# Kernel tuning notes

Measured on AMD Instinct MI355X. Metric: run time of the kernel, lower is better.

Reference implementation:

```python
import jax, jax.numpy as jnp
import numpy as np
import math

N, D_MODEL, H = 2048, 1024, 16
DK = D_MODEL // H
EPS = 1e-5


def setup_inputs() -> dict:
    key = jax.random.key(0)
    ks = jax.random.split(key, 10)
    s = 0.05  # scale to keep attention logits in a sane range
    return {
        "x": jax.random.normal(ks[0], (N, D_MODEL), jnp.float32),
        "wq": jax.random.normal(ks[1], (H * D_MODEL, DK), jnp.float32) * s,
        "q_bias": jax.random.normal(ks[2], (H, DK), jnp.float32) * s,
        "wk": jax.random.normal(ks[3], (H * D_MODEL, DK), jnp.float32) * s,
        "k_bias": jax.random.normal(ks[4], (H, DK), jnp.float32) * s,
        "wv": jax.random.normal(ks[5], (H * D_MODEL, DK), jnp.float32) * s,
        "v_bias": jax.random.normal(ks[6], (H, DK), jnp.float32) * s,
        "wo": jax.random.normal(ks[7], (D_MODEL, D_MODEL), jnp.float32) * s,
        "o_bias": jax.random.normal(ks[8], (D_MODEL,), jnp.float32) * s,
        "alpha": jnp.ones((D_MODEL,), jnp.float32),
        "beta": jnp.zeros((D_MODEL,), jnp.float32),
        "n": N,
        "d_model": D_MODEL,
        "h": H,
    }


def reference(x, wq, q_bias, wk, k_bias, wv, v_bias, wo, o_bias, alpha, beta, n, d_model, h):
    dk = d_model // h
    # per-head weight slices wq[i*d_model:(i+1)*d_model] -> [h, d_model, dk]
    wq3 = wq.reshape(h, d_model, dk)
    wk3 = wk.reshape(h, d_model, dk)
    wv3 = wv.reshape(h, d_model, dk)
    q = jnp.einsum('nd,hdk->hnk', x, wq3) + q_bias[:, None, :]  # [h,n,dk]
    k = jnp.einsum('nd,hdk->hnk', x, wk3) + k_bias[:, None, :]
    v = jnp.einsum('nd,hdk->hnk', x, wv3) + v_bias[:, None, :]
    scores = jnp.einsum('hnk,hmk->hnm', q, k) / math.sqrt(dk)  # [h,n,n]
    attn = jax.nn.softmax(scores, axis=-1)  # dim=1 of 2D [n,n] == last dim
    heads = jnp.einsum('hnm,hmk->hnk', attn, v)  # [h,n,dk]
    concat = heads.transpose(1, 0, 2).reshape(n, d_model)  # [n, d_model]
    out = concat @ wo + o_bias + x  # out-proj + residual
    mu = jnp.mean(out, axis=-1, keepdims=True)
    var = jnp.mean(jnp.square(out - mu), axis=-1, keepdims=True)
    return alpha * (out - mu) / jnp.sqrt(var + EPS) + beta
```

## Files before the change

kernel.cpp:

```cpp
#include <hip/hip_runtime.h>


#define NN 2048
#define DM 1024
#define NH 16
#define DKH 64

typedef __attribute__((ext_vector_type(4))) float f32x4;
typedef __attribute__((ext_vector_type(8))) __bf16 bf16x8;
typedef __attribute__((ext_vector_type(4))) __bf16 bf16x4;

#define AS1 __attribute__((address_space(1)))
#define AS3 __attribute__((address_space(3)))
#define GLOAD16(g, l) __builtin_amdgcn_global_load_lds((const AS1 void*)(g), (AS3 void*)(l), 16, 0, 0)

static __device__ __forceinline__ f32x4 mfma16(bf16x8 a, bf16x8 b, f32x4 c) {
  return __builtin_amdgcn_mfma_f32_16x16x32_bf16(a, b, c, 0, 0, 0);
}

static __device__ __forceinline__ bf16x8 cat44(bf16x4 a, bf16x4 b) {
  bf16x8 r;
  r[0] = a[0]; r[1] = a[1]; r[2] = a[2]; r[3] = a[3];
  r[4] = b[0]; r[5] = b[1]; r[6] = b[2]; r[7] = b[3];
  return r;
}

__global__ __launch_bounds__(256) void cvt_all(const float* __restrict__ x,
                                               const float* __restrict__ wq,
                                               const float* __restrict__ wk,
                                               const float* __restrict__ wv,
                                               const float* __restrict__ wo,
                                               __bf16* __restrict__ x_bf,
                                               __bf16* __restrict__ wqkv_t,
                                               __bf16* __restrict__ wo_t) {
  const int b = blockIdx.x, t = threadIdx.x;
  if (b < 1024) {
    int i = (b * 256 + t) * 8;
    float4 a = *(const float4*)(x + i);
    float4 c = *(const float4*)(x + i + 4);
    bf16x8 o;
    o[0] = (__bf16)a.x; o[1] = (__bf16)a.y; o[2] = (__bf16)a.z; o[3] = (__bf16)a.w;
    o[4] = (__bf16)c.x; o[5] = (__bf16)c.y; o[6] = (__bf16)c.z; o[7] = (__bf16)c.w;
    *(bf16x8*)(x_bf + i) = o;
  } else if (b < 2560) {
    int bb = b - 1024;
    int c = (bb % 12) * 256 + t;
    int oct = bb / 12;
    const float* src = (c < 1024) ? wq : (c < 2048 ? wk : wv);
    int hk = c & 1023;
    int hh = hk >> 6, dkk = hk & 63;
    bf16x8 o;
#pragma unroll
    for (int j = 0; j < 8; ++j)
      o[j] = (__bf16)src[(hh * 1024 + oct * 8 + j) * 64 + dkk];
    *(bf16x8*)(wqkv_t + c * 1024 + oct * 8) = o;
  } else {
    int bb = b - 2560;
    int c = (bb % 4) * 256 + t;
    int oct = bb / 4;
    bf16x8 o;
#pragma unroll
    for (int j = 0; j < 8; ++j)
      o[j] = (__bf16)wo[(oct * 8 + j) * 1024 + c];
    *(bf16x8*)(wo_t + c * 1024 + oct * 8) = o;
  }
}

__global__ __launch_bounds__(256) void gemm_qkv(const __bf16* __restrict__ A,
                                                const __bf16* __restrict__ Bt,
                                                const float* __restrict__ biasq,
                                                const float* __restrict__ biask,
                                                const float* __restrict__ biasv,
                                                __bf16* __restrict__ Qo,
                                                __bf16* __restrict__ Ko,
                                                __bf16* __restrict__ Vto) {
  __shared__ __align__(16) __bf16 Al[2][128 * 32];
  __shared__ __align__(16) __bf16 Bl[2][128 * 32];
  const int t = threadIdx.x;
  const int w = t >> 6, lane = t & 63, l15 = lane & 15, g = lane >> 4;
  const int bb = blockIdx.x;
  const int xk = bb & 7, s = bb >> 3;
  const int bx = (xk & 3) * 6 + s % 6;
  const int by = (xk >> 2) * 8 + s / 6;
  const int m0 = by * 128, n0 = bx * 128;
  const int wr = (w >> 1) * 64, wc = (w & 1) * 64;

  f32x4 acc[4][4] = {};

#define STAGE_QKV(buf, k0v)                                                      \
  do {                                                                           \
    _Pragma("unroll") for (int i = 0; i < 2; ++i) {                              \
      int L = (w * 2 + i) * 64 + lane;                                           \
      int row = L >> 2, kc = L & 3;                                              \
      GLOAD16(A + (m0 + row) * DM + (k0v) + kc * 8,                              \
              (char*)Al + (buf) * 8192 + (w * 2 + i) * 1024);                    \
      GLOAD16(Bt + (n0 + row) * DM + (k0v) + kc * 8,                             \
              (char*)Bl + (buf) * 8192 + (w * 2 + i) * 1024);                    \
    }                                                                            \
  } while (0)

  STAGE_QKV(0, 0);
  __syncthreads();
  int cur = 0;
  for (int k0 = 0; k0 < DM; k0 += 32) {
    if (k0 + 32 < DM) STAGE_QKV(cur ^ 1, k0 + 32);
    const char* Ab = (const char*)Al + cur * 8192;
    const char* Bb = (const char*)Bl + cur * 8192;
    bf16x8 af[4], bfv[4];
#pragma unroll
    for (int mf = 0; mf < 4; ++mf)
      af[mf] = *(const bf16x8*)(Ab + (wr + mf * 16 + l15) * 64 + g * 16);
#pragma unroll
    for (int nf = 0; nf < 4; ++nf)
      bfv[nf] = *(const bf16x8*)(Bb + (wc + nf * 16 + l15) * 64 + g * 16);
#pragma unroll
    for (int mf = 0; mf < 4; ++mf)
#pragma unroll
      for (int nf = 0; nf < 4; ++nf)
        acc[mf][nf] = mfma16(af[mf], bfv[nf], acc[mf][nf]);
    __syncthreads();
    cur ^= 1;
  }

  const int mtx = n0 >> 10;
  if (mtx == 0) {
#pragma unroll
    for (int nf = 0; nf < 4; ++nf) {
      int hk = (n0 & 1023) + wc + nf * 16 + l15;
      int hh = hk >> 6, dkk = hk & 63;
      float bias = biasq[hk];
#pragma unroll
      for (int mf = 0; mf < 4; ++mf)
#pragma unroll
        for (int r = 0; r < 4; ++r) {
          int n = m0 + wr + mf * 16 + g * 4 + r;
          Qo[(hh * NN + n) * DKH + dkk] = (__bf16)((acc[mf][nf][r] + bias) * 0.18033688f);
        }
    }
  } else if (mtx == 1) {
#pragma unroll
    for (int nf = 0; nf < 4; ++nf) {
      int hk = (n0 & 1023) + wc + nf * 16 + l15;
      int hh = hk >> 6, dkk = hk & 63;
      float bias = biask[hk];
#pragma unroll
      for (int mf = 0; mf < 4; ++mf)
#pragma unroll
        for (int r = 0; r < 4; ++r) {
          int n = m0 + wr + mf * 16 + g * 4 + r;
          Ko[(hh * NN + n) * DKH + dkk] = (__bf16)(acc[mf][nf][r] + bias);
        }
    }
  } else {
#pragma unroll
    for (int nf = 0; nf < 4; ++nf) {
      int hk = (n0 & 1023) + wc + nf * 16 + l15;
      int hh = hk >> 6, dkk = hk & 63;
      float bias = biasv[hk];
#pragma unroll
      for (int mf = 0; mf < 4; ++mf) {
        int nb = m0 + wr + mf * 16 + g * 4;
        int bl = nb & 127;
        int pcol = (nb & ~127) + ((bl >> 5) << 5) + (((bl >> 2) & 3) << 3) +
                   (((bl >> 4) & 1) << 2);
        bf16x4 pk;
#pragma unroll
        for (int r = 0; r < 4; ++r) pk[r] = (__bf16)(acc[mf][nf][r] + bias);
        *(bf16x4*)(Vto + hh * (DKH * NN) + dkk * NN + pcol) = pk;
      }
    }
  }
}

__global__ __launch_bounds__(256, 1) void attn_kernel(const __bf16* __restrict__ Qg,
                                                      const __bf16* __restrict__ Kg,
                                                      const __bf16* __restrict__ Vtg,
                                                      __bf16* __restrict__ Og) {
  __shared__ __align__(16) char Kl[2][16384];
  __shared__ __align__(16) char Vl[2][16384];
  const int t = threadIdx.x;
  const int w = t >> 6, lane = t & 63, l15 = lane & 15, g = lane >> 4;
  const int b = blockIdx.x;
  const int h = (b & 7) * 2 + ((b >> 3) >> 4);
  const int qb0 = ((b >> 3) & 15) * 128;

  const int rA = qb0 + w * 32 + l15;
  const __bf16* qpA = Qg + (h * NN + rA) * DKH + g * 8;
  bf16x8 qfA0 = *(const bf16x8*)qpA;
  bf16x8 qfA1 = *(const bf16x8*)(qpA + 32);
  const __bf16* qpB = qpA + 16 * DKH;
  bf16x8 qfB0 = *(const bf16x8*)qpB;
  bf16x8 qfB1 = *(const bf16x8*)(qpB + 32);

  f32x4 oaccA[4] = {}, oaccB[4] = {};
  float lsA = 0.f, lsB = 0.f;

#define STAGE_ATTN(buf, kbv)                                                     \
  do {                                                                           \
    _Pragma("unroll") for (int i = 0; i < 4; ++i) {                              \
      int L = i * 256 + t;                                                       \
      int rk = L >> 3, ok = (L & 7) ^ (rk & 7);                                  \
      GLOAD16(Kg + (h * NN + (kbv) + rk) * DKH + ok * 8, Kl[buf] + L * 16);      \
    }                                                                            \
    _Pragma("unroll") for (int i = 0; i < 4; ++i) {                              \
      int L = i * 256 + t;                                                       \
      int rv = L >> 4, ov = (L & 15) ^ (rv & 7);                                 \
      GLOAD16(Vtg + h * (DKH * NN) + rv * NN + (kbv) + ov * 8, Vl[buf] + L * 16);\
    }                                                                            \
  } while (0)

  STAGE_ATTN(0, 0);
  __syncthreads();
  int cur = 0;
  const int swz = (l15 & 7) << 4;
  for (int kb = 0; kb < NN; kb += 128) {
    if (kb + 128 < NN) STAGE_ATTN(cur ^ 1, kb + 128);

    bf16x4 pkA[8], pkB[8];
#pragma unroll
    for (int h2 = 0; h2 < 8; ++h2) {
      const char* kbase = Kl[cur] + (h2 * 16 + l15) * 128;
      bf16x8 kf0 = *(const bf16x8*)(kbase + ((g * 16) ^ swz));
      bf16x8 kf1 = *(const bf16x8*)(kbase + ((64 + g * 16) ^ swz));
      f32x4 zA = {};
      zA = mfma16(kf0, qfA0, zA);
      zA = mfma16(kf1, qfA1, zA);
      f32x4 zB = {};
      zB = mfma16(kf0, qfB0, zB);
      zB = mfma16(kf1, qfB1, zB);
      float a0 = exp2f(zA[0]), a1 = exp2f(zA[1]), a2 = exp2f(zA[2]), a3 = exp2f(zA[3]);
      lsA += (a0 + a1) + (a2 + a3);
      pkA[h2][0] = (__bf16)a0; pkA[h2][1] = (__bf16)a1;
      pkA[h2][2] = (__bf16)a2; pkA[h2][3] = (__bf16)a3;
      float b0 = exp2f(zB[0]), b1 = exp2f(zB[1]), b2 = exp2f(zB[2]), b3 = exp2f(zB[3]);
      lsB += (b0 + b1) + (b2 + b3);
      pkB[h2][0] = (__bf16)b0; pkB[h2][1] = (__bf16)b1;
      pkB[h2][2] = (__bf16)b2; pkB[h2][3] = (__bf16)b3;
    }

#pragma unroll
    for (int hp = 0; hp < 4; ++hp) {
      bf16x8 paA = cat44(pkA[2 * hp], pkA[2 * hp + 1]);
      bf16x8 paB = cat44(pkB[2 * hp], pkB[2 * hp + 1]);
#pragma unroll
      for (int cb = 0; cb < 4; ++cb) {
        int vrow = cb * 16 + l15;
        bf16x8 vv = *(const bf16x8*)(Vl[cur] + vrow * 256 +
                                     ((((4 * hp + g) ^ (vrow & 7))) << 4));
        oaccA[cb] = mfma16(paA, vv, oaccA[cb]);
        oaccB[cb] = mfma16(paB, vv, oaccB[cb]);
      }
    }
    __syncthreads();
    cur ^= 1;
  }

  float lrA = lsA; lrA += __shfl_xor(lrA, 16); lrA += __shfl_xor(lrA, 32);
  float lrB = lsB; lrB += __shfl_xor(lrB, 16); lrB += __shfl_xor(lrB, 32);
#pragma unroll
  for (int r = 0; r < 4; ++r) {
    float invA = 1.0f / __shfl(lrA, g * 4 + r);
    float invB = 1.0f / __shfl(lrB, g * 4 + r);
    int qA = qb0 + w * 32 + g * 4 + r;
#pragma unroll
    for (int cb = 0; cb < 4; ++cb) {
      Og[qA * DM + h * DKH + cb * 16 + l15] = (__bf16)(oaccA[cb][r] * invA);
      Og[(qA + 16) * DM + h * DKH + cb * 16 + l15] = (__bf16)(oaccB[cb][r] * invB);
    }
  }
}

__global__ __launch_bounds__(256) void gemm_proj(const __bf16* __restrict__ A,
                                                 const __bf16* __restrict__ Bt,
                                                 const float* __restrict__ obias,
                                                 const float* __restrict__ xres,
                                                 float* __restrict__ outp) {
  __shared__ __align__(16) __bf16 Al[2][128 * 32];
  __shared__ __align__(16) __bf16 Bl[2][64 * 32];
  const int t = threadIdx.x;
  const int w = t >> 6, lane = t & 63, l15 = lane & 15, g = lane >> 4;
  const int bb = blockIdx.x;
  const int xk = bb & 7, s = bb >> 3;
  const int bx = (xk & 3) * 4 + (s & 3);
  const int by = (xk >> 2) * 8 + (s >> 2);
  const int m0 = by * 128, n0 = bx * 64;

  f32x4 acc[2][4] = {};

#define STAGE_PROJ(buf, k0v)                                                     \
  do {                                                                           \
    _Pragma("unroll") for (int i = 0; i < 2; ++i) {                              \
      int L = (w * 2 + i) * 64 + lane;                                           \
      int row = L >> 2, kc = L & 3;                                              \
      GLOAD16(A + (m0 + row) * DM + (k0v) + kc * 8,                              \
              (char*)Al + (buf) * 8192 + (w * 2 + i) * 1024);                    \
    }                                                                            \
    {                                                                            \
      int L = w * 64 + lane;                                                     \
      int row = L >> 2, kc = L & 3;                                              \
      GLOAD16(Bt + (n0 + row) * DM + (k0v) + kc * 8,                             \
              (char*)Bl + (buf) * 4096 + w * 1024);                              \
    }                                                                            \
  } while (0)

  STAGE_PROJ(0, 0);
  __syncthreads();
  int cur = 0;
  for (int k0 = 0; k0 < DM; k0 += 32) {
    if (k0 + 32 < DM) STAGE_PROJ(cur ^ 1, k0 + 32);
    const char* Ab = (const char*)Al + cur * 8192;
    const char* Bb = (const char*)Bl + cur * 4096;
    bf16x8 af[2], bfv[4];
#pragma unroll
    for (int mf = 0; mf < 2; ++mf)
      af[mf] = *(const bf16x8*)(Ab + (w * 32 + mf * 16 + l15) * 64 + g * 16);
#pragma unroll
    for (int nf = 0; nf < 4; ++nf)
      bfv[nf] = *(const bf16x8*)(Bb + (nf * 16 + l15) * 64 + g * 16);
#pragma unroll
    for (int mf = 0; mf < 2; ++mf)
#pragma unroll
      for (int nf = 0; nf < 4; ++nf)
        acc[mf][nf] = mfma16(af[mf], bfv[nf], acc[mf][nf]);
    __syncthreads();
    cur ^= 1;
  }

#pragma unroll
  for (int nf = 0; nf < 4; ++nf) {
    int col = n0 + nf * 16 + l15;
    float ob = obias[col];
#pragma unroll
    for (int mf = 0; mf < 2; ++mf)
#pragma unroll
      for (int r = 0; r < 4; ++r) {
        int row = m0 + w * 32 + mf * 16 + g * 4 + r;
        outp[row * DM + col] = acc[mf][nf][r] + ob + xres[row * DM + col];
      }
  }
}

__global__ __launch_bounds__(256) void ln_kernel(const float* __restrict__ in,
                                                 const float* __restrict__ alpha,
                                                 const float* __restrict__ beta,
                                                 float* __restrict__ out) {
  const int row = blockIdx.x, t = threadIdx.x;
  const int lane = t & 63, w = t >> 6;
  float4 v = ((const float4*)(in + row * DM))[t];
  float s = v.x + v.y + v.z + v.w;
  float s2 = v.x * v.x + v.y * v.y + v.z * v.z + v.w * v.w;
#pragma unroll
  for (int off = 32; off >= 1; off >>= 1) {
    s += __shfl_xor(s, off);
    s2 += __shfl_xor(s2, off);
  }
  __shared__ float ps[8];
  if (lane == 0) { ps[w] = s; ps[4 + w] = s2; }
  __syncthreads();
  float S = ps[0] + ps[1] + ps[2] + ps[3];
  float S2 = ps[4] + ps[5] + ps[6] + ps[7];
  float mu = S * (1.0f / DM);
  float var = S2 * (1.0f / DM) - mu * mu;
  float rstd = rsqrtf(var + 1e-5f);
  float4 a = ((const float4*)alpha)[t];
  float4 b = ((const float4*)beta)[t];
  float4 o;
  o.x = a.x * (v.x - mu) * rstd + b.x;
  o.y = a.y * (v.y - mu) * rstd + b.y;
  o.z = a.z * (v.z - mu) * rstd + b.z;
  o.w = a.w * (v.w - mu) * rstd + b.w;
  ((float4*)(out + row * DM))[t] = o;
}

extern "C" void kernel_launch(void* const* d_in, const int* in_sizes, int n_in,
                              void* d_out, int out_size, void* d_ws, size_t ws_size,
                              hipStream_t stream) {
  const float* x     = (const float*)d_in[0];
  const float* wq    = (const float*)d_in[1];
  const float* qb    = (const float*)d_in[2];
  const float* wk    = (const float*)d_in[3];
  const float* kb    = (const float*)d_in[4];
  const float* wv    = (const float*)d_in[5];
  const float* vb    = (const float*)d_in[6];
  const float* wo    = (const float*)d_in[7];
  const float* ob    = (const float*)d_in[8];
  const float* alpha = (const float*)d_in[9];
  const float* beta  = (const float*)d_in[10];
  float* out = (float*)d_out;
  char* ws = (char*)d_ws;

  __bf16* x_bf   = (__bf16*)(ws);
  __bf16* wqkv_t = (__bf16*)(ws + (4ull << 20));
  __bf16* wo_t   = (__bf16*)(ws + (10ull << 20));
  __bf16* Qb     = (__bf16*)(ws + (12ull << 20));
  __bf16* Kb     = (__bf16*)(ws + (16ull << 20));
  __bf16* Vtb    = (__bf16*)(ws + (20ull << 20));
  __bf16* attn   = (__bf16*)(ws + (24ull << 20));
  float*  outp   = (float*)(ws + (28ull << 20));

  cvt_all<<<dim3(3072), dim3(256), 0, stream>>>(x, wq, wk, wv, wo, x_bf, wqkv_t, wo_t);
  gemm_qkv<<<dim3(384), dim3(256), 0, stream>>>(x_bf, wqkv_t, qb, kb, vb, Qb, Kb, Vtb);
  attn_kernel<<<dim3(256), dim3(256), 0, stream>>>(Qb, Kb, Vtb, attn);
  gemm_proj<<<dim3(256), dim3(256), 0, stream>>>(attn, wo_t, ob, x, outp);
  ln_kernel<<<dim3(2048), dim3(256), 0, stream>>>(outp, alpha, beta, out);
}
```

Measured before the change: 184.4 us.

## Split attention KV range across two blocks and add combine kernel

Splits each attention block's key/value sweep into two halves, doubling the grid from 256 to 512 blocks so the 256 CUs of the MI355X can hold more than one wave of work, and raises launch bounds to allow 2 blocks per CU. Partial unnormalized outputs and row sums are written in fp32 to workspace, and a new combine kernel sums the halves, normalizes, and writes bf16. This is safe without max-rescaling because the original already uses exp2 without max subtraction. It adds an extra kernel launch and about 16MB of fp32 partial traffic.

```diff
diff --git a/kernel.cpp b/kernel.cpp
--- a/kernel.cpp
+++ b/kernel.cpp
@@ -172,17 +172,21 @@
   }
 }
 
-__global__ __launch_bounds__(256, 1) void attn_kernel(const __bf16* __restrict__ Qg,
+__global__ __launch_bounds__(256, 2) void attn_kernel(const __bf16* __restrict__ Qg,
                                                       const __bf16* __restrict__ Kg,
                                                       const __bf16* __restrict__ Vtg,
-                                                      __bf16* __restrict__ Og) {
+                                                      float* __restrict__ Opart,
+                                                      float* __restrict__ lpart) {
   __shared__ __align__(16) char Kl[2][16384];
   __shared__ __align__(16) char Vl[2][16384];
   const int t = threadIdx.x;
   const int w = t >> 6, lane = t & 63, l15 = lane & 15, g = lane >> 4;
   const int b = blockIdx.x;
-  const int h = (b & 7) * 2 + ((b >> 3) >> 4);
-  const int qb0 = ((b >> 3) & 15) * 128;
+  const int loc = (b >> 3);
+  const int h = (b & 7) * 2 + (loc >> 5);
+  const int qb0 = ((loc & 31) >> 1) * 128;
+  const int half = loc & 1;
+  const int kv0 = half * 1024, kvend = kv0 + 1024;
 
   const int rA = qb0 + w * 32 + l15;
   const __bf16* qpA = Qg + (h * NN + rA) * DKH + g * 8;
@@ -209,12 +213,12 @@
     }                                                                            \
   } while (0)
 
-  STAGE_ATTN(0, 0);
+  STAGE_ATTN(0, kv0);
   __syncthreads();
   int cur = 0;
   const int swz = (l15 & 7) << 4;
-  for (int kb = 0; kb < NN; kb += 128) {
-    if (kb + 128 < NN) STAGE_ATTN(cur ^ 1, kb + 128);
+  for (int kb = kv0; kb < kvend; kb += 128) {
+    if (kb + 128 < kvend) STAGE_ATTN(cur ^ 1, kb + 128);
 
     bf16x4 pkA[8], pkB[8];
 #pragma unroll
@@ -257,17 +261,37 @@
 
   float lrA = lsA; lrA += __shfl_xor(lrA, 16); lrA += __shfl_xor(lrA, 32);
   float lrB = lsB; lrB += __shfl_xor(lrB, 16); lrB += __shfl_xor(lrB, 32);
+  if (g == 0) {
+    lpart[half * (NH * NN) + h * NN + qb0 + w * 32 + l15] = lrA;
+    lpart[half * (NH * NN) + h * NN + qb0 + w * 32 + 16 + l15] = lrB;
+  }
+  float* Ob = Opart + (size_t)half * (NN * DM);
 #pragma unroll
   for (int r = 0; r < 4; ++r) {
-    float invA = 1.0f / __shfl(lrA, g * 4 + r);
-    float invB = 1.0f / __shfl(lrB, g * 4 + r);
     int qA = qb0 + w * 32 + g * 4 + r;
 #pragma unroll
     for (int cb = 0; cb < 4; ++cb) {
-      Og[qA * DM + h * DKH + cb * 16 + l15] = (__bf16)(oaccA[cb][r] * invA);
-      Og[(qA + 16) * DM + h * DKH + cb * 16 + l15] = (__bf16)(oaccB[cb][r] * invB);
-    }
-  }
+      Ob[qA * DM + h * DKH + cb * 16 + l15] = oaccA[cb][r];
+      Ob[(qA + 16) * DM + h * DKH + cb * 16 + l15] = oaccB[cb][r];
+    }
+  }
+}
+
+__global__ __launch_bounds__(256) void attn_combine(const float* __restrict__ Opart,
+                                                    const float* __restrict__ lpart,
+                                                    __bf16* __restrict__ attn) {
+  const int q = blockIdx.x, t = threadIdx.x;
+  const int h = t >> 4, d4 = (t & 15) * 4;
+  const int idx = q * DM + h * DKH + d4;
+  float4 o0 = *(const float4*)(Opart + idx);
+  float4 o1 = *(const float4*)(Opart + NN * DM + idx);
+  float inv = 1.0f / (lpart[h * NN + q] + lpart[NH * NN + h * NN + q]);
+  bf16x4 r;
+  r[0] = (__bf16)((o0.x + o1.x) * inv);
+  r[1] = (__bf16)((o0.y + o1.y) * inv);
+  r[2] = (__bf16)((o0.z + o1.z) * inv);
+  r[3] = (__bf16)((o0.w + o1.w) * inv);
+  *(bf16x4*)(attn + idx) = r;
 }
 
 __global__ __launch_bounds__(256) void gemm_proj(const __bf16* __restrict__ A,
@@ -397,10 +421,13 @@
   __bf16* Vtb    = (__bf16*)(ws + (20ull << 20));
   __bf16* attn   = (__bf16*)(ws + (24ull << 20));
   float*  outp   = (float*)(ws + (28ull << 20));
+  float*  Opart  = (float*)(ws + (36ull << 20));
+  float*  lpart  = (float*)(ws + (52ull << 20));
 
   cvt_all<<<dim3(3072), dim3(256), 0, stream>>>(x, wq, wk, wv, wo, x_bf, wqkv_t, wo_t);
   gemm_qkv<<<dim3(384), dim3(256), 0, stream>>>(x_bf, wqkv_t, qb, kb, vb, Qb, Kb, Vtb);
-  attn_kernel<<<dim3(256), dim3(256), 0, stream>>>(Qb, Kb, Vtb, attn);
+  attn_kernel<<<dim3(512), dim3(256), 0, stream>>>(Qb, Kb, Vtb, Opart, lpart);
+  attn_combine<<<dim3(2048), dim3(256), 0, stream>>>(Opart, lpart, attn);
   gemm_proj<<<dim3(256), dim3(256), 0, stream>>>(attn, wo_t, ob, x, outp);
   ln_kernel<<<dim3(2048), dim3(256), 0, stream>>>(outp, alpha, beta, out);
 }
```

Result: no change. 181.4 us (-1.6%).
